# Optimization experiments

Measured on AMD Instinct MI355X. Metric: run time of the kernel, lower is better.

Reference implementation:

```python
import jax, jax.numpy as jnp
import numpy as np

L, N, C, F, H = 6, 16384, 8, 128, 128


def setup_inputs() -> dict:
    key = jax.random.key(0)
    ks = jax.random.split(key, 8)
    node_features = jax.random.normal(ks[0], (L, N, F), dtype=jnp.float32)
    # child indices point into the hidden states of the level below
    child_idx = jax.random.randint(ks[1], (L, N, C), 0, N)
    # random child masks; bottom level (processed first) has no children (leaves)
    child_mask = jax.random.randint(ks[2], (L, N, C), 0, 2).astype(bool)
    child_mask = child_mask.at[L - 1].set(False)
    A_c = jax.random.uniform(ks[3], (L, N, C, C), dtype=jnp.float32)
    s = 1.0 / np.sqrt(H)
    W_g = jax.random.normal(ks[4], (H, H), dtype=jnp.float32) * s
    W_ih = jax.random.normal(ks[5], (F, H), dtype=jnp.float32) * s
    W_hh = jax.random.normal(ks[6], (H, H), dtype=jnp.float32) * s
    b_ih = jnp.zeros((H,), dtype=jnp.float32)
    b_hh = jnp.zeros((H,), dtype=jnp.float32)
    return {
        "node_features": node_features, "child_idx": child_idx,
        "child_mask": child_mask, "A_c": A_c,
        "W_g": W_g, "W_ih": W_ih, "W_hh": W_hh,
        "b_ih": b_ih, "b_hh": b_hh,
    }


def reference(node_features, child_idx, child_mask, A_c, W_g, W_ih, W_hh, b_ih, b_hh):
    # Level-wise (bottom-up) batched form of deepFirstConvolution:
    #   gather child hiddens -> edge graph conv -> masked maxpool readout -> RNN update
    neg = jnp.finfo(node_features.dtype).min

    def step(h_below, level):  # h_below: [N, H]
        x, cidx, cmask, a = level
        ch = h_below[cidx] * cmask[..., None]              # [N, C, H] gather + zero-pad
        g = jax.nn.relu(jnp.einsum('ncd,ndh->nch', a, ch) @ W_g)  # edge graph conv
        pooled = jnp.where(cmask[..., None], g, neg).max(axis=1)  # maxpool readout [N, H]
        has_child = cmask.any(axis=1, keepdims=True)
        pooled = jnp.where(has_child, pooled, 0.0)         # leaves get zero init hiddens
        h_new = jnp.tanh(x @ W_ih + b_ih + pooled @ W_hh + b_hh)  # RNN update
        return h_new, None

    # process from deepest level (index L-1) up to the root level (index 0)
    levels = (node_features[::-1], child_idx[::-1], child_mask[::-1], A_c[::-1])
    h0 = jnp.zeros((node_features.shape[1], W_hh.shape[0]), dtype=node_features.dtype)
    root_hiddens, _ = jax.lax.scan(step, h0, levels)
    return root_hiddens  # [N, H]
```

## Files before the change

kernel.cpp:

```cpp
#include <hip/hip_runtime.h>
#include <cfloat>

#define LL 6
#define NN 16384
#define CC 8
#define FF 128
#define HH 128
#define BN 16

typedef __bf16 bf16x8 __attribute__((ext_vector_type(8)));
typedef __attribute__((ext_vector_type(4))) float f32x4;

static __device__ inline unsigned short f2bfbits(float f) {
    return __builtin_bit_cast(unsigned short, (__bf16)f);
}
static __device__ inline float bfbits2f(unsigned short b) {
    return (float)__builtin_bit_cast(__bf16, b);
}
static __device__ inline float fast_tanh(float x) {
    const float e = __expf(2.0f * x);
    return 1.0f - __fdividef(2.0f, e + 1.0f);
}

#define SWZ(row, byte) ((unsigned)(((row) * 256 + (byte)) ^ (((row) & 7) << 4)))

__device__ inline unsigned char make_maskbyte(const unsigned char* raw,
                                              int n, int f_i32) {
    if (f_i32) {
        const uint4 v0 = *(const uint4*)(raw + (size_t)n * 32);
        const uint4 v1 = *(const uint4*)(raw + (size_t)n * 32 + 16);
        return (v0.x ? 1 : 0) | (v0.y ? 2 : 0) | (v0.z ? 4 : 0) | (v0.w ? 8 : 0)
             | (v1.x ? 16 : 0) | (v1.y ? 32 : 0) | (v1.z ? 64 : 0) | (v1.w ? 128 : 0);
    } else {
        const unsigned a = *(const unsigned*)(raw + (size_t)n * 8);
        const unsigned c = *(const unsigned*)(raw + (size_t)n * 8 + 4);
        return ((a & 0xFFu) ? 1 : 0) | ((a & 0xFF00u) ? 2 : 0)
             | ((a & 0xFF0000u) ? 4 : 0) | ((a >> 24) ? 8 : 0)
             | ((c & 0xFFu) ? 16 : 0) | ((c & 0xFF00u) ? 32 : 0)
             | ((c & 0xFF0000u) ? 64 : 0) | ((c >> 24) ? 128 : 0);
    }
}

__global__ __launch_bounds__(256) void prologue_kernel(
    const unsigned char* __restrict__ mask_raw,
    const float* __restrict__ Wg, const float* __restrict__ Wih,
    const float* __restrict__ Whh,
    const float* __restrict__ bih, const float* __restrict__ bhh,
    unsigned char* __restrict__ mbits,
    unsigned short* __restrict__ WgHi, unsigned short* __restrict__ WgLo,
    unsigned short* __restrict__ WdHi, unsigned short* __restrict__ WdLo,
    float* __restrict__ bias) {
    __shared__ int s_any;
    const int tid = threadIdx.x;
    if (tid == 0) s_any = 0;
    __syncthreads();
    {
        const unsigned a = ((const unsigned*)mask_raw)[tid * 2 + 0];
        const unsigned b = ((const unsigned*)mask_raw)[tid * 2 + 1];
        if (((a | b) & 0xFFFFFF00u) != 0) atomicOr(&s_any, 1);
    }
    __syncthreads();
    const int f_i32 = s_any ? 0 : 1;

    const int g = blockIdx.x * 256 + tid;
    if (g < LL * NN) mbits[g] = make_maskbyte(mask_raw, g, f_i32);

    if (g < 2048) {
        const int l = g & 63;
        const int nt = g >> 8;
        const int kt = (g >> 6) & 3;
        const int n = nt * 16 + (l & 15);
        const int kb = kt * 32 + (l >> 4) * 8;
        #pragma unroll
        for (int i = 0; i < 8; ++i) {
            const float v = Wg[(kb + i) * HH + n];
            const unsigned short hb = f2bfbits(v);
            WgHi[g * 8 + i] = hb;
            WgLo[g * 8 + i] = f2bfbits(v - bfbits2f(hb));
        }
    } else if (g < 6144) {
        const int u = g - 2048;
        const int l = u & 63;
        const int nt = u >> 9;
        const int kt = (u >> 6) & 7;
        const int n = nt * 16 + (l & 15);
        const int kb = (kt & 3) * 32 + (l >> 4) * 8;
        const float* W = (kt < 4) ? Wih : Whh;
        #pragma unroll
        for (int i = 0; i < 8; ++i) {
            const float v = W[(kb + i) * HH + n];
            const unsigned short hb = f2bfbits(v);
            WdHi[u * 8 + i] = hb;
            WdLo[u * 8 + i] = f2bfbits(v - bfbits2f(hb));
        }
    } else if (g < 6272) {
        const int n = g - 6144;
        bias[n] = bih[n] + bhh[n];
    }
}

__global__ __launch_bounds__(256) void level_kernel(
    const float* __restrict__ x_l, const int* __restrict__ cidx_l,
    const unsigned char* __restrict__ mbits_l,
    const float* __restrict__ Hp_in, const float* __restrict__ a_l,
    const unsigned short* __restrict__ WgHi, const unsigned short* __restrict__ WgLo,
    const unsigned short* __restrict__ WdHi, const unsigned short* __restrict__ WdLo,
    const float* __restrict__ bias,
    float* __restrict__ h_out,
    float* __restrict__ Hp_out)
{
    __shared__ __align__(16) unsigned char pH[BN * 256];
    __shared__ __align__(16) unsigned char pL[BN * 256];
    __shared__ float a_lds[BN][CC][CC];
    __shared__ int   cidx_lds[BN][CC];
    __shared__ __align__(16) unsigned char maskbyte[BN];

    const int tid = threadIdx.x;
    const int lane = tid & 63;
    const int w = tid >> 6;
    const int lrow = lane & 15, lgrp = lane >> 4;
    const long nbase = (long)blockIdx.x * BN;

    ((float4*)a_lds)[tid] = ((const float4*)(a_l + nbase * CC * CC))[tid];
    if (tid < 32)
        ((uint4*)cidx_lds)[tid] = ((const uint4*)(cidx_l + nbase * CC))[tid];
    if (tid < BN) maskbyte[tid] = mbits_l[nbase + tid];
    __syncthreads();

    const uint4 mball = *(const uint4*)maskbyte;
    const int any = (mball.x | mball.y | mball.z | mball.w) != 0;

    if (any) {
        for (int nl = 0; nl < 4; ++nl) {
            const int node = w * 4 + nl;
            const int mb = maskbyte[node];
            float m0 = 0.f, m1 = 0.f;
            if (mb) {
                float c0[CC], c1[CC];
                #pragma unroll
                for (int c = 0; c < CC; ++c) { c0[c] = 0.f; c1[c] = 0.f; }
                #pragma unroll
                for (int c = 0; c < CC; ++c) {
                    if (mb & (1 << c)) {
                        const float2 v = *(const float2*)&Hp_in[(size_t)cidx_lds[node][c] * HH + 2 * lane];
                        c0[c] = v.x; c1[c] = v.y;
                    }
                }
                float mm0 = -FLT_MAX, mm1 = -FLT_MAX;
                #pragma unroll
                for (int c = 0; c < CC; ++c) {
                    if (mb & (1 << c)) {
                        float s0 = 0.f, s1 = 0.f;
                        #pragma unroll
                        for (int d = 0; d < CC; ++d) {
                            const float av = a_lds[node][c][d];
                            s0 += av * c0[d]; s1 += av * c1[d];
                        }
                        mm0 = fmaxf(mm0, fmaxf(s0, 0.f));
                        mm1 = fmaxf(mm1, fmaxf(s1, 0.f));
                    }
                }
                m0 = mm0; m1 = mm1;
            }
            const unsigned short h0 = f2bfbits(m0);
            const unsigned short h1 = f2bfbits(m1);
            const unsigned short l0 = f2bfbits(m0 - bfbits2f(h0));
            const unsigned short l1 = f2bfbits(m1 - bfbits2f(h1));
            const unsigned off = SWZ(node, lane * 4);
            *(unsigned*)&pH[off] = (unsigned)h0 | ((unsigned)h1 << 16);
            *(unsigned*)&pL[off] = (unsigned)l0 | ((unsigned)l1 << 16);
        }
        __syncthreads();
    }

    bf16x8 ah[8], al[8];
    #pragma unroll
    for (int kt = 0; kt < 4; ++kt) {
        const float* src = &x_l[(nbase + lrow) * FF + kt * 32 + lgrp * 8];
        const float4 v0 = *(const float4*)src;
        const float4 v1 = *(const float4*)(src + 4);
        const float vv[8] = {v0.x, v0.y, v0.z, v0.w, v1.x, v1.y, v1.z, v1.w};
        bf16x8 hfr, lfr;
        #pragma unroll
        for (int i = 0; i < 8; ++i) {
            const __bf16 hb = (__bf16)vv[i];
            hfr[i] = hb;
            lfr[i] = (__bf16)(vv[i] - (float)hb);
        }
        ah[kt] = hfr; al[kt] = lfr;
    }
    if (any) {
        #pragma unroll
        for (int kt = 4; kt < 8; ++kt) {
            const unsigned off = SWZ(lrow, (kt - 4) * 64 + lgrp * 16);
            ah[kt] = *(const bf16x8*)&pH[off];
            al[kt] = *(const bf16x8*)&pL[off];
        }
    }
    float hv[2][4];
    #pragma unroll
    for (int nn = 0; nn < 2; ++nn) {
        const int nt = w * 2 + nn;
        f32x4 acc = {0.f, 0.f, 0.f, 0.f};
        #pragma unroll
        for (int kt = 0; kt < 4; ++kt) {
            const bf16x8 bh = *(const bf16x8*)&WdHi[((nt * 8 + kt) * 64 + lane) * 8];
            const bf16x8 bl = *(const bf16x8*)&WdLo[((nt * 8 + kt) * 64 + lane) * 8];
            acc = __builtin_amdgcn_mfma_f32_16x16x32_bf16(ah[kt], bh, acc, 0, 0, 0);
            acc = __builtin_amdgcn_mfma_f32_16x16x32_bf16(ah[kt], bl, acc, 0, 0, 0);
            acc = __builtin_amdgcn_mfma_f32_16x16x32_bf16(al[kt], bh, acc, 0, 0, 0);
        }
        if (any) {
            #pragma unroll
            for (int kt = 4; kt < 8; ++kt) {
                const bf16x8 bh = *(const bf16x8*)&WdHi[((nt * 8 + kt) * 64 + lane) * 8];
                const bf16x8 bl = *(const bf16x8*)&WdLo[((nt * 8 + kt) * 64 + lane) * 8];
                acc = __builtin_amdgcn_mfma_f32_16x16x32_bf16(ah[kt], bh, acc, 0, 0, 0);
                acc = __builtin_amdgcn_mfma_f32_16x16x32_bf16(ah[kt], bl, acc, 0, 0, 0);
                acc = __builtin_amdgcn_mfma_f32_16x16x32_bf16(al[kt], bh, acc, 0, 0, 0);
            }
        }
        const float b = bias[nt * 16 + lrow];
        #pragma unroll
        for (int r = 0; r < 4; ++r)
            hv[nn][r] = fast_tanh(acc[r] + b);
    }

    if (h_out != nullptr) {
        #pragma unroll
        for (int nn = 0; nn < 2; ++nn) {
            const int nt = w * 2 + nn;
            #pragma unroll
            for (int r = 0; r < 4; ++r)
                h_out[(nbase + lgrp * 4 + r) * HH + nt * 16 + lrow] = hv[nn][r];
        }
    }
    if (Hp_out != nullptr) {
        __syncthreads();
        #pragma unroll
        for (int nn = 0; nn < 2; ++nn) {
            #pragma unroll
            for (int r = 0; r < 4; ++r) {
                const int row = lgrp * 4 + r;
                const int col = (w * 2 + nn) * 16 + lrow;
                const unsigned short hb = f2bfbits(hv[nn][r]);
                const unsigned short lb = f2bfbits(hv[nn][r] - bfbits2f(hb));
                const unsigned off = SWZ(row, col * 2);
                *(unsigned short*)&pH[off] = hb;
                *(unsigned short*)&pL[off] = lb;
            }
        }
        __syncthreads();
        bf16x8 aHh[4], aLh[4];
        #pragma unroll
        for (int kt = 0; kt < 4; ++kt) {
            const unsigned off = SWZ(lrow, kt * 64 + lgrp * 16);
            aHh[kt] = *(const bf16x8*)&pH[off];
            aLh[kt] = *(const bf16x8*)&pL[off];
        }
        #pragma unroll
        for (int nn = 0; nn < 2; ++nn) {
            const int nt = w * 2 + nn;
            f32x4 acc = {0.f, 0.f, 0.f, 0.f};
            #pragma unroll
            for (int kt = 0; kt < 4; ++kt) {
                const bf16x8 bh = *(const bf16x8*)&WgHi[((nt * 4 + kt) * 64 + lane) * 8];
                const bf16x8 bl = *(const bf16x8*)&WgLo[((nt * 4 + kt) * 64 + lane) * 8];
                acc = __builtin_amdgcn_mfma_f32_16x16x32_bf16(aHh[kt], bh, acc, 0, 0, 0);
                acc = __builtin_amdgcn_mfma_f32_16x16x32_bf16(aHh[kt], bl, acc, 0, 0, 0);
                acc = __builtin_amdgcn_mfma_f32_16x16x32_bf16(aLh[kt], bh, acc, 0, 0, 0);
            }
            #pragma unroll
            for (int r = 0; r < 4; ++r)
                Hp_out[(nbase + lgrp * 4 + r) * HH + nt * 16 + lrow] = acc[r];
        }
    }
}

extern "C" void kernel_launch(void* const* d_in, const int* in_sizes, int n_in,
                              void* d_out, int out_size, void* d_ws, size_t ws_size,
                              hipStream_t stream) {
    const float* nf   = (const float*)d_in[0];
    const int*   cidx = (const int*)d_in[1];
    const unsigned char* mraw = (const unsigned char*)d_in[2];
    const float* A_c  = (const float*)d_in[3];
    const float* Wg   = (const float*)d_in[4];
    const float* Wih  = (const float*)d_in[5];
    const float* Whh  = (const float*)d_in[6];
    const float* bih  = (const float*)d_in[7];
    const float* bhh  = (const float*)d_in[8];
    float* outp = (float*)d_out;

    char* ws = (char*)d_ws;
    unsigned char* mbits = (unsigned char*)ws;
    unsigned short* WgHi = (unsigned short*)(ws + (128 << 10));
    unsigned short* WgLo = (unsigned short*)(ws + (160 << 10));
    unsigned short* WdHi = (unsigned short*)(ws + (192 << 10));
    unsigned short* WdLo = (unsigned short*)(ws + (256 << 10));
    float* bias          = (float*)(ws + (320 << 10));
    float* HpA           = (float*)(ws + (1 << 20));
    float* HpB           = (float*)(ws + (1 << 20) + (8 << 20));

    prologue_kernel<<<(LL * NN) / 256, 256, 0, stream>>>(
        mraw, Wg, Wih, Whh, bih, bhh, mbits, WgHi, WgLo, WdHi, WdLo, bias);

    for (int s = 0; s < LL; ++s) {
        const int l = LL - 1 - s;
        float* hp_in  = (s & 1) ? HpB : HpA;
        float* hp_out = (s & 1) ? HpA : HpB;
        level_kernel<<<NN / BN, 256, 0, stream>>>(
            nf   + (size_t)l * NN * FF,
            cidx + (size_t)l * NN * CC,
            mbits + (size_t)l * NN,
            hp_in,
            A_c  + (size_t)l * NN * CC * CC,
            WgHi, WgLo, WdHi, WdLo, bias,
            (s == LL - 1) ? outp : nullptr,
            (s == LL - 1) ? nullptr : hp_out);
    }
}
```

Baseline: 139.2 us.

## Prefetch node features early and interleave child gathers for two nodes

Moves the global loads of node features to the start of the kernel so they overlap the LDS staging and child gather phase. It also processes two nodes per pass instead of one, so the dependent gather loads for both nodes are in flight together and memory-level parallelism rises. The launch bounds gain a minimum of 4 blocks per CU, which caps register use to protect occupancy. The 32 extra live registers for the prefetched features, plus doubled gather buffers, raise register pressure and may cause spills under the new cap.

After: 131.2 us. 1.06x faster.

```diff
diff --git a/kernel.cpp b/kernel.cpp
--- a/kernel.cpp
+++ b/kernel.cpp
@@ -99,7 +99,7 @@
     }
 }
 
-__global__ __launch_bounds__(256) void level_kernel(
+__global__ __launch_bounds__(256, 4) void level_kernel(
     const float* __restrict__ x_l, const int* __restrict__ cidx_l,
     const unsigned char* __restrict__ mbits_l,
     const float* __restrict__ Hp_in, const float* __restrict__ a_l,
@@ -121,6 +121,14 @@
     const int lrow = lane & 15, lgrp = lane >> 4;
     const long nbase = (long)blockIdx.x * BN;
 
+    float4 xr[8];
+    #pragma unroll
+    for (int kt = 0; kt < 4; ++kt) {
+        const float* src = &x_l[(nbase + lrow) * FF + kt * 32 + lgrp * 8];
+        xr[kt * 2 + 0] = *(const float4*)src;
+        xr[kt * 2 + 1] = *(const float4*)(src + 4);
+    }
+
     ((float4*)a_lds)[tid] = ((const float4*)(a_l + nbase * CC * CC))[tid];
     if (tid < 32)
         ((uint4*)cidx_lds)[tid] = ((const uint4*)(cidx_l + nbase * CC))[tid];
@@ -131,44 +139,81 @@
     const int any = (mball.x | mball.y | mball.z | mball.w) != 0;
 
     if (any) {
-        for (int nl = 0; nl < 4; ++nl) {
-            const int node = w * 4 + nl;
-            const int mb = maskbyte[node];
-            float m0 = 0.f, m1 = 0.f;
-            if (mb) {
-                float c0[CC], c1[CC];
-                #pragma unroll
-                for (int c = 0; c < CC; ++c) { c0[c] = 0.f; c1[c] = 0.f; }
+        #pragma unroll
+        for (int pass = 0; pass < 2; ++pass) {
+            const int nodeA = w * 4 + pass * 2;
+            const int nodeB = nodeA + 1;
+            const int mbA = maskbyte[nodeA];
+            const int mbB = maskbyte[nodeB];
+            float a0[CC], a1[CC], b0[CC], b1[CC];
+            #pragma unroll
+            for (int c = 0; c < CC; ++c) {
+                a0[c] = 0.f; a1[c] = 0.f; b0[c] = 0.f; b1[c] = 0.f;
+            }
+            #pragma unroll
+            for (int c = 0; c < CC; ++c) {
+                if (mbA & (1 << c)) {
+                    const float2 v = *(const float2*)&Hp_in[(size_t)cidx_lds[nodeA][c] * HH + 2 * lane];
+                    a0[c] = v.x; a1[c] = v.y;
+                }
+                if (mbB & (1 << c)) {
+                    const float2 v = *(const float2*)&Hp_in[(size_t)cidx_lds[nodeB][c] * HH + 2 * lane];
+                    b0[c] = v.x; b1[c] = v.y;
+                }
+            }
+            float mA0 = 0.f, mA1 = 0.f, mB0 = 0.f, mB1 = 0.f;
+            if (mbA) {
+                float m0 = -FLT_MAX, m1 = -FLT_MAX;
                 #pragma unroll
                 for (int c = 0; c < CC; ++c) {
-                    if (mb & (1 << c)) {
-                        const float2 v = *(const float2*)&Hp_in[(size_t)cidx_lds[node][c] * HH + 2 * lane];
-                        c0[c] = v.x; c1[c] = v.y;
-                    }
-                }
-                float mm0 = -FLT_MAX, mm1 = -FLT_MAX;
-                #pragma unroll
-                for (int c = 0; c < CC; ++c) {
-                    if (mb & (1 << c)) {
+                    if (mbA & (1 << c)) {
                         float s0 = 0.f, s1 = 0.f;
                         #pragma unroll
                         for (int d = 0; d < CC; ++d) {
-                            const float av = a_lds[node][c][d];
-                            s0 += av * c0[d]; s1 += av * c1[d];
+                            const float av = a_lds[nodeA][c][d];
+                            s0 += av * a0[d]; s1 += av * a1[d];
                         }
-                        mm0 = fmaxf(mm0, fmaxf(s0, 0.f));
-                        mm1 = fmaxf(mm1, fmaxf(s1, 0.f));
+                        m0 = fmaxf(m0, fmaxf(s0, 0.f));
+                        m1 = fmaxf(m1, fmaxf(s1, 0.f));
                     }
                 }
-                m0 = mm0; m1 = mm1;
-            }
-            const unsigned short h0 = f2bfbits(m0);
-            const unsigned short h1 = f2bfbits(m1);
-            const unsigned short l0 = f2bfbits(m0 - bfbits2f(h0));
-            const unsigned short l1 = f2bfbits(m1 - bfbits2f(h1));
-            const unsigned off = SWZ(node, lane * 4);
-            *(unsigned*)&pH[off] = (unsigned)h0 | ((unsigned)h1 << 16);
-            *(unsigned*)&pL[off] = (unsigned)l0 | ((unsigned)l1 << 16);
+                mA0 = m0; mA1 = m1;
+            }
+            if (mbB) {
+                float m0 = -FLT_MAX, m1 = -FLT_MAX;
+                #pragma unroll
+                for (int c = 0; c < CC; ++c) {
+                    if (mbB & (1 << c)) {
+                        float s0 = 0.f, s1 = 0.f;
+                        #pragma unroll
+                        for (int d = 0; d < CC; ++d) {
+                            const float av = a_lds[nodeB][c][d];
+                            s0 += av * b0[d]; s1 += av * b1[d];
+                        }
+                        m0 = fmaxf(m0, fmaxf(s0, 0.f));
+                        m1 = fmaxf(m1, fmaxf(s1, 0.f));
+                    }
+                }
+                mB0 = m0; mB1 = m1;
+            }
+            {
+                const unsigned short h0 = f2bfbits(mA0);
+                const unsigned short h1 = f2bfbits(mA1);
+                const unsigned short l0 = f2bfbits(mA0 - bfbits2f(h0));
+                const unsigned short l1 = f2bfbits(mA1 - bfbits2f(h1));
+                const unsigned off = SWZ(nodeA, lane * 4);
+                *(unsigned*)&pH[off] = (unsigned)h0 | ((unsigned)h1 << 16);
+                *(unsigned*)&pL[off] = (unsigned)l0 | ((unsigned)l1 << 16);
+            }
+            {
+                const unsigned short h0 = f2bfbits(mB0);
+                const unsigned short h1 = f2bfbits(mB1);
+                const unsigned short l0 = f2bfbits(mB0 - bfbits2f(h0));
+                const unsigned short l1 = f2bfbits(mB1 - bfbits2f(h1));
+                const unsigned off = SWZ(nodeB, lane * 4);
+                *(unsigned*)&pH[off] = (unsigned)h0 | ((unsigned)h1 << 16);
+                *(unsigned*)&pL[off] = (unsigned)l0 | ((unsigned)l1 << 16);
+            }
         }
         __syncthreads();
     }
@@ -176,9 +221,8 @@
     bf16x8 ah[8], al[8];
     #pragma unroll
     for (int kt = 0; kt < 4; ++kt) {
-        const float* src = &x_l[(nbase + lrow) * FF + kt * 32 + lgrp * 8];
-        const float4 v0 = *(const float4*)src;
-        const float4 v1 = *(const float4*)(src + 4);
+        const float4 v0 = xr[kt * 2 + 0];
+        const float4 v1 = xr[kt * 2 + 1];
         const float vv[8] = {v0.x, v0.y, v0.z, v0.w, v1.x, v1.y, v1.z, v1.w};
         bf16x8 hfr, lfr;
         #pragma unroll
```
